# Kernel tuning notes

Measured on AMD Instinct MI355X. Metric: run time of the kernel, lower is better.

## Reference

```python
import jax, jax.numpy as jnp
import numpy as np

# Static problem configuration
NUM_GRAPHS = 64
NODES_PER_GRAPH = 2048          # divisible by OUT_H
NODE_EMB_DIM = 256              # divisible by OUT_W
COND_EMB_DIM = 64
OUT_H, OUT_W = 16, 8            # AdaptiveAvgPool2d output -> pooled dim H*W = 128
MLP_H = 256
BN_EPS = 1e-5


def setup_inputs() -> dict:
    key = jax.random.key(0)
    ks = jax.random.split(key, 8)
    N = NUM_GRAPHS * NODES_PER_GRAPH
    x = jax.random.normal(ks[0], (N, NODE_EMB_DIM), dtype=jnp.float32)
    # equal contiguous segments: node i belongs to graph i // NODES_PER_GRAPH
    batch = jnp.repeat(jnp.arange(NUM_GRAPHS, dtype=jnp.int64), NODES_PER_GRAPH)
    conditioner_z_ref = jax.random.normal(ks[1], (N, COND_EMB_DIM), dtype=jnp.float32)
    mlp_in = COND_EMB_DIM + OUT_H * OUT_W
    W1 = jax.random.normal(ks[2], (mlp_in, MLP_H), dtype=jnp.float32) / np.sqrt(mlp_in)
    b1 = jnp.zeros((MLP_H,), dtype=jnp.float32)
    gamma = jnp.ones((MLP_H,), dtype=jnp.float32)
    beta = jnp.zeros((MLP_H,), dtype=jnp.float32)
    W2 = jax.random.normal(ks[3], (MLP_H, 3), dtype=jnp.float32) / np.sqrt(MLP_H)
    b2 = jnp.zeros((3,), dtype=jnp.float32)
    return {"x": x, "batch": batch, "conditioner_z_ref": conditioner_z_ref,
            "W1": W1, "b1": b1, "gamma": gamma, "beta": beta, "W2": W2, "b2": b2}


def _adaptive_pool(x):
    # x: [N_total, D] with equal contiguous segments of NODES_PER_GRAPH rows per graph.
    # AdaptiveAvgPool2d((OUT_H, OUT_W)) on each [n, D] "image"; since n % OUT_H == 0
    # and D % OUT_W == 0 the adaptive bins are uniform -> exact reshape-mean.
    B = x.shape[0] // NODES_PER_GRAPH
    xg = x.reshape(B, OUT_H, NODES_PER_GRAPH // OUT_H, OUT_W, NODE_EMB_DIM // OUT_W)
    pooled = xg.mean(axis=(2, 4))                 # [B, OUT_H, OUT_W]
    return pooled.reshape(B, OUT_H * OUT_W)       # [B, H*W]


def reference(x, batch, conditioner_z_ref, W1, b1, gamma, beta, W2, b2):
    batch_pooled = _adaptive_pool(x)                          # [B, H*W]
    gathered = batch_pooled[batch]                            # [N, H*W]
    h = jnp.concatenate([conditioner_z_ref, gathered], axis=1)  # [N, cond + H*W]
    # Linear -> BatchNorm1d (training-mode batch stats, biased var) -> GELU (exact)
    h = h @ W1 + b1                                           # [N, MLP_H]
    mean = h.mean(axis=0)
    var = h.var(axis=0)
    h = (h - mean) * jax.lax.rsqrt(var + BN_EPS) * gamma + beta
    h = jax.nn.gelu(h, approximate=False)
    return h @ W2 + b2                                        # [N, 3]
```

## Files before the change

### kernel.cpp

```cpp
#include <hip/hip_runtime.h>
#include <math.h>

#define NG    64
#define NPG   2048
#define NTOT  (NG*NPG)
#define ZD    64
#define PD    128
#define MH    256

typedef __attribute__((ext_vector_type(8))) short bf16x8;
typedef __attribute__((ext_vector_type(4))) float f32x4;

__device__ __forceinline__ unsigned short f2bf(float f){
  unsigned u = __float_as_uint(f);
  unsigned r = u + 0x7FFFu + ((u >> 16) & 1u);
  return (unsigned short)(r >> 16);
}
__device__ __forceinline__ float bf2f(unsigned short s){
  return __uint_as_float(((unsigned)s) << 16);
}
__device__ __forceinline__ float gelu_f(float x){
  float u = x * x;
  float a = fmaf(0.044715f, u, 1.0f);
  float e = __builtin_amdgcn_exp2f(-2.3022083f * x * a);
  return x * __builtin_amdgcn_rcpf(1.0f + e);
}

__launch_bounds__(256)
__global__ void k1_pool_zstat(const float* __restrict__ x, const float* __restrict__ z,
                              float* __restrict__ pooled, float* __restrict__ St,
                              float* __restrict__ C){
  __shared__ __align__(16) unsigned short s_zt[64 * 264];
  __shared__ float s_cred[4096];
  int tid = threadIdx.x;

  if (blockIdx.x >= 256){
    int bi = blockIdx.x - 256;
    int b  = bi >> 4;
    int oh = bi & 15;
    int c4 = tid & 63;
    int rq = tid >> 6;
    const float4* x4 = (const float4*)x;
    size_t base = (size_t)(b * NPG + oh * 128) * 64;
    float4 acc = make_float4(0.f, 0.f, 0.f, 0.f);
    #pragma unroll 8
    for (int i = 0; i < 32; i++){
      float4 v = x4[base + (size_t)(rq + i * 4) * 64 + c4];
      acc.x += v.x; acc.y += v.y; acc.z += v.z; acc.w += v.w;
    }
    s_cred[tid] = acc.x + acc.y + acc.z + acc.w;
    __syncthreads();
    if (tid < 8){
      float s = 0.f;
      #pragma unroll
      for (int w = 0; w < 4; w++)
        #pragma unroll
        for (int j = 0; j < 8; j++)
          s += s_cred[w * 64 + tid * 8 + j];
      pooled[b * PD + oh * 8 + tid] = s * (1.0f / 4096.0f);
    }
    return;
  }

  int blk = blockIdx.x;
  int g = blk >> 2, q4 = blk & 3;
  int lane = tid & 63, wave = tid >> 6;
  int col = lane & 15, quad = lane >> 4;
  const float4* z4 = (const float4*)z + ((size_t)g * 2048 + q4 * 512) * 16;
  int d4 = col;
  int mg = quad;

  f32x4 acc[4][4];
  #pragma unroll
  for (int a = 0; a < 4; a++)
    #pragma unroll
    for (int b = 0; b < 4; b++) acc[a][b] = (f32x4)(0.f);
  float s0 = 0.f, s1 = 0.f, s2 = 0.f, s3 = 0.f;

  for (int ch = 0; ch < 2; ch++){
    #pragma unroll
    for (int rd = 0; rd < 4; rd++){
      int m0 = rd * 64 + wave * 16 + mg * 4;
      const float4* src = z4 + ch * 4096 + m0 * 16 + d4;
      float4 v0 = src[0];
      float4 v1 = src[16];
      float4 v2 = src[32];
      float4 v3 = src[48];
      s0 += v0.x + v1.x + v2.x + v3.x;
      s1 += v0.y + v1.y + v2.y + v3.y;
      s2 += v0.z + v1.z + v2.z + v3.z;
      s3 += v0.w + v1.w + v2.w + v3.w;
      int slot = m0 >> 3;
      int sub  = m0 & 4;
      int d0 = d4 * 4;
      {
        int d = d0 + 0; int ss = slot ^ ((d >> 3) & 7);
        ushort4 w = make_ushort4(f2bf(v0.x), f2bf(v1.x), f2bf(v2.x), f2bf(v3.x));
        *(ushort4*)&s_zt[d * 264 + ss * 8 + sub] = w;
      }
      {
        int d = d0 + 1; int ss = slot ^ ((d >> 3) & 7);
        ushort4 w = make_ushort4(f2bf(v0.y), f2bf(v1.y), f2bf(v2.y), f2bf(v3.y));
        *(ushort4*)&s_zt[d * 264 + ss * 8 + sub] = w;
      }
      {
        int d = d0 + 2; int ss = slot ^ ((d >> 3) & 7);
        ushort4 w = make_ushort4(f2bf(v0.z), f2bf(v1.z), f2bf(v2.z), f2bf(v3.z));
        *(ushort4*)&s_zt[d * 264 + ss * 8 + sub] = w;
      }
      {
        int d = d0 + 3; int ss = slot ^ ((d >> 3) & 7);
        ushort4 w = make_ushort4(f2bf(v0.w), f2bf(v1.w), f2bf(v2.w), f2bf(v3.w));
        *(ushort4*)&s_zt[d * 264 + ss * 8 + sub] = w;
      }
    }
    __syncthreads();
    #pragma unroll
    for (int ks = 0; ks < 2; ks++){
      bf16x8 fr[4];
      #pragma unroll
      for (int t = 0; t < 4; t++){
        int row = t * 16 + col;
        int ss  = (wave * 8 + ks * 4 + quad) ^ ((row >> 3) & 7);
        fr[t] = *(const bf16x8*)&s_zt[row * 264 + ss * 8];
      }
      #pragma unroll
      for (int mt = 0; mt < 4; mt++)
        #pragma unroll
        for (int nt = 0; nt < 4; nt++)
          acc[mt][nt] = __builtin_amdgcn_mfma_f32_16x16x32_bf16(fr[mt], fr[nt], acc[mt][nt], 0, 0, 0);
    }
    __syncthreads();
  }

  s0 += __shfl_xor(s0, 16); s0 += __shfl_xor(s0, 32);
  s1 += __shfl_xor(s1, 16); s1 += __shfl_xor(s1, 32);
  s2 += __shfl_xor(s2, 16); s2 += __shfl_xor(s2, 32);
  s3 += __shfl_xor(s3, 16); s3 += __shfl_xor(s3, 32);
  if (quad == 0){
    atomicAdd(&St[(d4 * 4 + 0) * 64 + g], s0);
    atomicAdd(&St[(d4 * 4 + 1) * 64 + g], s1);
    atomicAdd(&St[(d4 * 4 + 2) * 64 + g], s2);
    atomicAdd(&St[(d4 * 4 + 3) * 64 + g], s3);
  }

  #pragma unroll
  for (int w = 0; w < 4; w++){
    if (wave == w){
      #pragma unroll
      for (int mt = 0; mt < 4; mt++)
        #pragma unroll
        for (int nt = 0; nt < 4; nt++)
          #pragma unroll
          for (int r = 0; r < 4; r++){
            int p = mt * 16 + quad * 4 + r;
            int qc = nt * 16 + col;
            if (w == 0) s_cred[p * 64 + qc]  = acc[mt][nt][r];
            else        s_cred[p * 64 + qc] += acc[mt][nt][r];
          }
    }
    __syncthreads();
  }
  for (int f = tid; f < 4096; f += 256)
    atomicAdd(&C[f], s_cred[f]);
}

__launch_bounds__(256)
__global__ void k2_stats(const float* __restrict__ pooled, const float* __restrict__ W1,
                         const float* __restrict__ b1, const float* __restrict__ gamma,
                         const float* __restrict__ beta, const float* __restrict__ C,
                         const float* __restrict__ St, float* __restrict__ Aj,
                         float* __restrict__ cprime, unsigned short* __restrict__ Wbf){
  __shared__ float pl[64 * 129];
  int tid = threadIdx.x;
  int jc = tid >> 6, lane = tid & 63;
  int j = blockIdx.x * 4 + jc;

  Wbf[(size_t)j * 64 + lane] = f2bf(W1[(size_t)lane * 256 + j]);

  for (int idx = tid; idx < 8192; idx += 256)
    pl[(idx >> 7) * 129 + (idx & 127)] = pooled[idx];
  __syncthreads();

  float g = b1[j];
  #pragma unroll 8
  for (int k = 0; k < 128; k++)
    g = fmaf(pl[lane * 129 + k], W1[(size_t)(ZD + k) * MH + j], g);

  float wl = W1[(size_t)lane * MH + j];
  float t1 = 0.f, t2 = 0.f;
  #pragma unroll
  for (int q = 0; q < 64; q++){
    float wq = __uint_as_float(__builtin_amdgcn_readlane(__float_as_uint(wl), q));
    t1 = fmaf(C [q * 64 + lane], wq, t1);
    t2 = fmaf(St[q * 64 + lane], wq, t2);
  }
  float v_wcw = wl * t1;
  float v_gs  = g * t2;
  float v_s   = t2;
  float v_g   = g;
  float v_g2  = g * g;
  #pragma unroll
  for (int off = 32; off; off >>= 1){
    v_wcw += __shfl_xor(v_wcw, off);
    v_gs  += __shfl_xor(v_gs , off);
    v_s   += __shfl_xor(v_s  , off);
    v_g   += __shfl_xor(v_g  , off);
    v_g2  += __shfl_xor(v_g2 , off);
  }
  const float invN = 1.0f / (float)NTOT;
  float mean = v_s * invN + v_g * (1.0f / 64.0f);
  float eh2  = v_wcw * invN + 2.0f * invN * v_gs + v_g2 * (1.0f / 64.0f);
  float var  = eh2 - mean * mean;
  float aj = gamma[j] * rsqrtf(var + 1e-5f);
  if (lane == 0) Aj[j] = aj;
  cprime[lane * MH + j] = fmaf(aj, g, beta[j] - aj * mean);
}

__launch_bounds__(256, 2)
__global__ void final_kernel(const float* __restrict__ z, const unsigned short* __restrict__ Wbf,
                             const float* __restrict__ Aj, const float* __restrict__ cp,
                             const float* __restrict__ W2, const float* __restrict__ b2,
                             float* __restrict__ out){
  __shared__ __align__(16) unsigned short zt[128 * 136];
  __shared__ float slab[2][384];
  int tid = threadIdx.x;
  int n0 = blockIdx.x * 128;
  int g = blockIdx.x >> 4;

  const float4* z4 = (const float4*)z + (size_t)n0 * 16;
  #pragma unroll
  for (int i = 0; i < 8; i++){
    int idx = tid + i * 256;
    int m = idx >> 4, d4 = idx & 15;
    float4 v = z4[idx];
    ushort4 h, l;
    h.x = f2bf(v.x); l.x = f2bf(v.x - bf2f(h.x));
    h.y = f2bf(v.y); l.y = f2bf(v.y - bf2f(h.y));
    h.z = f2bf(v.z); l.z = f2bf(v.z - bf2f(h.z));
    h.w = f2bf(v.w); l.w = f2bf(v.w - bf2f(h.w));
    *(ushort4*)&zt[m * 136 + d4 * 4]      = h;
    *(ushort4*)&zt[m * 136 + 64 + d4 * 4] = l;
  }
  __syncthreads();

  int lane = tid & 63, wave = tid >> 6;
  int wm = wave & 1, wn = wave >> 1;
  int col = lane & 15, quad = lane >> 4;
  int mbase = wm * 64, nbase = wn * 128;

  f32x4 acc[4][8];
  #pragma unroll
  for (int mt = 0; mt < 4; mt++)
    #pragma unroll
    for (int nt = 0; nt < 8; nt++) acc[mt][nt] = (f32x4)(0.f);

  #pragma unroll
  for (int ks = 0; ks < 4; ks++){
    int k0 = ks * 32;
    bf16x8 af[4];
    #pragma unroll
    for (int mt = 0; mt < 4; mt++)
      af[mt] = *(const bf16x8*)&zt[(mbase + mt * 16 + col) * 136 + k0 + quad * 8];
    #pragma unroll
    for (int nt = 0; nt < 8; nt++){
      bf16x8 bv = *(const bf16x8*)&Wbf[(size_t)(nbase + nt * 16 + col) * 64 + (ks & 1) * 32 + quad * 8];
      #pragma unroll
      for (int mt = 0; mt < 4; mt++)
        acc[mt][nt] = __builtin_amdgcn_mfma_f32_16x16x32_bf16(af[mt], bv, acc[mt][nt], 0, 0, 0);
    }
  }

  float aj[8], cj[8], w2a[8], w2b[8], w2c[8];
  #pragma unroll
  for (int nt = 0; nt < 8; nt++){
    int j = nbase + nt * 16 + col;
    aj[nt] = Aj[j];
    cj[nt] = cp[g * MH + j];
    w2a[nt] = W2[j * 3 + 0];
    w2b[nt] = W2[j * 3 + 1];
    w2c[nt] = W2[j * 3 + 2];
  }

  #pragma unroll
  for (int mt = 0; mt < 4; mt++){
    #pragma unroll
    for (int r = 0; r < 4; r++){
      float o0 = 0.f, o1 = 0.f, o2 = 0.f;
      #pragma unroll
      for (int nt = 0; nt < 8; nt++){
        float h  = fmaf(aj[nt], acc[mt][nt][r], cj[nt]);
        float ge = gelu_f(h);
        o0 = fmaf(ge, w2a[nt], o0);
        o1 = fmaf(ge, w2b[nt], o1);
        o2 = fmaf(ge, w2c[nt], o2);
      }
      #pragma unroll
      for (int off = 8; off; off >>= 1){
        o0 += __shfl_xor(o0, off);
        o1 += __shfl_xor(o1, off);
        o2 += __shfl_xor(o2, off);
      }
      if (col == 0){
        int node = mbase + mt * 16 + quad * 4 + r;
        slab[wn][node * 3 + 0] = o0;
        slab[wn][node * 3 + 1] = o1;
        slab[wn][node * 3 + 2] = o2;
      }
    }
  }
  __syncthreads();
  float b2v[3] = {b2[0], b2[1], b2[2]};
  for (int f = tid; f < 384; f += 256)
    out[(size_t)blockIdx.x * 384 + f] = slab[0][f] + slab[1][f] + b2v[f % 3];
}

extern "C" void kernel_launch(void* const* d_in, const int* in_sizes, int n_in,
                              void* d_out, int out_size, void* d_ws, size_t ws_size,
                              hipStream_t stream){
  (void)in_sizes; (void)n_in; (void)out_size; (void)ws_size;
  const float* x     = (const float*)d_in[0];
  const float* z     = (const float*)d_in[2];
  const float* W1    = (const float*)d_in[3];
  const float* b1    = (const float*)d_in[4];
  const float* gamma = (const float*)d_in[5];
  const float* beta  = (const float*)d_in[6];
  const float* W2    = (const float*)d_in[7];
  const float* b2    = (const float*)d_in[8];
  float* out = (float*)d_out;

  float* W = (float*)d_ws;
  float* pooled = W;
  float* St     = W + 8192;
  float* C      = W + 12288;
  float* Aj     = W + 16384;
  float* CP     = W + 16640;
  unsigned short* Wbf = (unsigned short*)(W + 33024);

  hipMemsetAsync((char*)d_ws + 8192 * 4, 0, 8192 * 4, stream);

  k1_pool_zstat<<<dim3(1280), dim3(256), 0, stream>>>(x, z, pooled, St, C);
  k2_stats     <<<dim3(64),   dim3(256), 0, stream>>>(pooled, W1, b1, gamma, beta, C, St, Aj, CP, Wbf);
  final_kernel <<<dim3(NTOT / 128), dim3(256), 0, stream>>>(z, Wbf, Aj, CP, W2, b2, out);
}
```

Baseline: 271.9 us.

## Fuse all stages into one cooperative persistent kernel with grid syncs

Replaces the memset plus three kernel launches with a single cooperative kernel of 512 blocks that zeroes accumulators, computes pooling and z statistics, derives BN coefficients, and runs the final MLP/GELU pass, separated by grid-wide syncs. It is meant to remove launch overhead and inter-kernel gaps. The final stage becomes a persistent loop over row tiles. The old path is kept as a fallback if the cooperative launch fails. Grid syncs, reduced parallelism per phase (only 64 blocks in the stats phase) and occupancy limits from the large shared buffer may offset the gains.

```diff
diff --git a/kernel.cpp b/kernel.cpp
--- a/kernel.cpp
+++ b/kernel.cpp
@@ -1,5 +1,8 @@
 #include <hip/hip_runtime.h>
+#include <hip/hip_cooperative_groups.h>
 #include <math.h>
+
+namespace cg = cooperative_groups;
 
 #define NG    64
 #define NPG   2048
@@ -24,6 +27,311 @@
   float a = fmaf(0.044715f, u, 1.0f);
   float e = __builtin_amdgcn_exp2f(-2.3022083f * x * a);
   return x * __builtin_amdgcn_rcpf(1.0f + e);
+}
+
+__launch_bounds__(256, 2)
+__global__ void fused_all(const float* __restrict__ x, const float* __restrict__ z,
+                          const float* __restrict__ W1, const float* __restrict__ b1,
+                          const float* __restrict__ gamma, const float* __restrict__ beta,
+                          const float* __restrict__ W2, const float* __restrict__ b2,
+                          float* __restrict__ pooled, float* __restrict__ St,
+                          float* __restrict__ C, float* __restrict__ Aj,
+                          float* __restrict__ cp, unsigned short* __restrict__ Wbf,
+                          float* __restrict__ out){
+  __shared__ __align__(16) unsigned char smem[50176];
+  cg::grid_group gg = cg::this_grid();
+  int tid = threadIdx.x;
+  int bid = blockIdx.x;
+  int nb  = gridDim.x;
+
+  if (bid < 32){
+    int i = bid * 256 + tid;
+    if (i < 4096) St[i] = 0.f;
+    else          C[i - 4096] = 0.f;
+  }
+  gg.sync();
+
+  {
+    unsigned short* s_zt = (unsigned short*)smem;
+    float* s_cred = (float*)(smem + 33792);
+
+    if (bid < 256){
+      int blk = bid;
+      int g = blk >> 2, q4 = blk & 3;
+      int lane = tid & 63, wave = tid >> 6;
+      int col = lane & 15, quad = lane >> 4;
+      const float4* z4 = (const float4*)z + ((size_t)g * 2048 + q4 * 512) * 16;
+      int d4 = col;
+      int mg = quad;
+
+      f32x4 acc[4][4];
+      #pragma unroll
+      for (int a = 0; a < 4; a++)
+        #pragma unroll
+        for (int b = 0; b < 4; b++) acc[a][b] = (f32x4)(0.f);
+      float s0 = 0.f, s1 = 0.f, s2 = 0.f, s3 = 0.f;
+
+      for (int ch = 0; ch < 2; ch++){
+        #pragma unroll
+        for (int rd = 0; rd < 4; rd++){
+          int m0 = rd * 64 + wave * 16 + mg * 4;
+          const float4* src = z4 + ch * 4096 + m0 * 16 + d4;
+          float4 v0 = src[0];
+          float4 v1 = src[16];
+          float4 v2 = src[32];
+          float4 v3 = src[48];
+          s0 += v0.x + v1.x + v2.x + v3.x;
+          s1 += v0.y + v1.y + v2.y + v3.y;
+          s2 += v0.z + v1.z + v2.z + v3.z;
+          s3 += v0.w + v1.w + v2.w + v3.w;
+          int slot = m0 >> 3;
+          int sub  = m0 & 4;
+          int d0 = d4 * 4;
+          {
+            int d = d0 + 0; int ss = slot ^ ((d >> 3) & 7);
+            ushort4 w = make_ushort4(f2bf(v0.x), f2bf(v1.x), f2bf(v2.x), f2bf(v3.x));
+            *(ushort4*)&s_zt[d * 264 + ss * 8 + sub] = w;
+          }
+          {
+            int d = d0 + 1; int ss = slot ^ ((d >> 3) & 7);
+            ushort4 w = make_ushort4(f2bf(v0.y), f2bf(v1.y), f2bf(v2.y), f2bf(v3.y));
+            *(ushort4*)&s_zt[d * 264 + ss * 8 + sub] = w;
+          }
+          {
+            int d = d0 + 2; int ss = slot ^ ((d >> 3) & 7);
+            ushort4 w = make_ushort4(f2bf(v0.z), f2bf(v1.z), f2bf(v2.z), f2bf(v3.z));
+            *(ushort4*)&s_zt[d * 264 + ss * 8 + sub] = w;
+          }
+          {
+            int d = d0 + 3; int ss = slot ^ ((d >> 3) & 7);
+            ushort4 w = make_ushort4(f2bf(v0.w), f2bf(v1.w), f2bf(v2.w), f2bf(v3.w));
+            *(ushort4*)&s_zt[d * 264 + ss * 8 + sub] = w;
+          }
+        }
+        __syncthreads();
+        #pragma unroll
+        for (int ks = 0; ks < 2; ks++){
+          bf16x8 fr[4];
+          #pragma unroll
+          for (int t = 0; t < 4; t++){
+            int row = t * 16 + col;
+            int ss  = (wave * 8 + ks * 4 + quad) ^ ((row >> 3) & 7);
+            fr[t] = *(const bf16x8*)&s_zt[row * 264 + ss * 8];
+          }
+          #pragma unroll
+          for (int mt = 0; mt < 4; mt++)
+            #pragma unroll
+            for (int nt = 0; nt < 4; nt++)
+              acc[mt][nt] = __builtin_amdgcn_mfma_f32_16x16x32_bf16(fr[mt], fr[nt], acc[mt][nt], 0, 0, 0);
+        }
+        __syncthreads();
+      }
+
+      s0 += __shfl_xor(s0, 16); s0 += __shfl_xor(s0, 32);
+      s1 += __shfl_xor(s1, 16); s1 += __shfl_xor(s1, 32);
+      s2 += __shfl_xor(s2, 16); s2 += __shfl_xor(s2, 32);
+      s3 += __shfl_xor(s3, 16); s3 += __shfl_xor(s3, 32);
+      if (quad == 0){
+        atomicAdd(&St[(d4 * 4 + 0) * 64 + g], s0);
+        atomicAdd(&St[(d4 * 4 + 1) * 64 + g], s1);
+        atomicAdd(&St[(d4 * 4 + 2) * 64 + g], s2);
+        atomicAdd(&St[(d4 * 4 + 3) * 64 + g], s3);
+      }
+
+      #pragma unroll
+      for (int w = 0; w < 4; w++){
+        if (wave == w){
+          #pragma unroll
+          for (int mt = 0; mt < 4; mt++)
+            #pragma unroll
+            for (int nt = 0; nt < 4; nt++)
+              #pragma unroll
+              for (int r = 0; r < 4; r++){
+                int p = mt * 16 + quad * 4 + r;
+                int qc = nt * 16 + col;
+                if (w == 0) s_cred[p * 64 + qc]  = acc[mt][nt][r];
+                else        s_cred[p * 64 + qc] += acc[mt][nt][r];
+              }
+        }
+        __syncthreads();
+      }
+      for (int f = tid; f < 4096; f += 256)
+        atomicAdd(&C[f], s_cred[f]);
+    }
+
+    int u0 = bid, nu = (bid < 256) ? 1 : 3;
+    for (int k = 0; k < nu; k++){
+      int bi = u0 + k * 256;
+      int b  = bi >> 4;
+      int oh = bi & 15;
+      int c4 = tid & 63;
+      int rq = tid >> 6;
+      const float4* x4 = (const float4*)x;
+      size_t base = (size_t)(b * NPG + oh * 128) * 64;
+      float4 acc = make_float4(0.f, 0.f, 0.f, 0.f);
+      #pragma unroll 8
+      for (int i = 0; i < 32; i++){
+        float4 v = x4[base + (size_t)(rq + i * 4) * 64 + c4];
+        acc.x += v.x; acc.y += v.y; acc.z += v.z; acc.w += v.w;
+      }
+      __syncthreads();
+      s_cred[tid] = acc.x + acc.y + acc.z + acc.w;
+      __syncthreads();
+      if (tid < 8){
+        float s = 0.f;
+        #pragma unroll
+        for (int w = 0; w < 4; w++)
+          #pragma unroll
+          for (int j = 0; j < 8; j++)
+            s += s_cred[w * 64 + tid * 8 + j];
+        pooled[b * PD + oh * 8 + tid] = s * (1.0f / 4096.0f);
+      }
+    }
+  }
+  gg.sync();
+
+  if (bid < 64){
+    float* pl = (float*)smem;
+    int jc = tid >> 6, lane = tid & 63;
+    int j = bid * 4 + jc;
+
+    Wbf[(size_t)j * 64 + lane] = f2bf(W1[(size_t)lane * 256 + j]);
+
+    for (int idx = tid; idx < 8192; idx += 256)
+      pl[(idx >> 7) * 129 + (idx & 127)] = pooled[idx];
+    __syncthreads();
+
+    float g = b1[j];
+    #pragma unroll 8
+    for (int k = 0; k < 128; k++)
+      g = fmaf(pl[lane * 129 + k], W1[(size_t)(ZD + k) * MH + j], g);
+
+    float wl = W1[(size_t)lane * MH + j];
+    float t1 = 0.f, t2 = 0.f;
+    #pragma unroll
+    for (int q = 0; q < 64; q++){
+      float wq = __uint_as_float(__builtin_amdgcn_readlane(__float_as_uint(wl), q));
+      t1 = fmaf(C [q * 64 + lane], wq, t1);
+      t2 = fmaf(St[q * 64 + lane], wq, t2);
+    }
+    float v_wcw = wl * t1;
+    float v_gs  = g * t2;
+    float v_s   = t2;
+    float v_g   = g;
+    float v_g2  = g * g;
+    #pragma unroll
+    for (int off = 32; off; off >>= 1){
+      v_wcw += __shfl_xor(v_wcw, off);
+      v_gs  += __shfl_xor(v_gs , off);
+      v_s   += __shfl_xor(v_s  , off);
+      v_g   += __shfl_xor(v_g  , off);
+      v_g2  += __shfl_xor(v_g2 , off);
+    }
+    const float invN = 1.0f / (float)NTOT;
+    float mean = v_s * invN + v_g * (1.0f / 64.0f);
+    float eh2  = v_wcw * invN + 2.0f * invN * v_gs + v_g2 * (1.0f / 64.0f);
+    float var  = eh2 - mean * mean;
+    float aj = gamma[j] * rsqrtf(var + 1e-5f);
+    if (lane == 0) Aj[j] = aj;
+    cp[lane * MH + j] = fmaf(aj, g, beta[j] - aj * mean);
+  }
+  gg.sync();
+
+  {
+    unsigned short* zt = (unsigned short*)smem;
+    float* slab = (float*)(smem + 34816);
+    int lane = tid & 63, wave = tid >> 6;
+    int wm = wave & 1, wn = wave >> 1;
+    int col = lane & 15, quad = lane >> 4;
+    int mbase = wm * 64, nbase = wn * 128;
+
+    for (int u = bid; u < 1024; u += nb){
+      int n0 = u * 128;
+      int g = u >> 4;
+
+      const float4* z4 = (const float4*)z + (size_t)n0 * 16;
+      __syncthreads();
+      #pragma unroll
+      for (int i = 0; i < 8; i++){
+        int idx = tid + i * 256;
+        int m = idx >> 4, d4 = idx & 15;
+        float4 v = z4[idx];
+        ushort4 h, l;
+        h.x = f2bf(v.x); l.x = f2bf(v.x - bf2f(h.x));
+        h.y = f2bf(v.y); l.y = f2bf(v.y - bf2f(h.y));
+        h.z = f2bf(v.z); l.z = f2bf(v.z - bf2f(h.z));
+        h.w = f2bf(v.w); l.w = f2bf(v.w - bf2f(h.w));
+        *(ushort4*)&zt[m * 136 + d4 * 4]      = h;
+        *(ushort4*)&zt[m * 136 + 64 + d4 * 4] = l;
+      }
+      __syncthreads();
+
+      f32x4 acc[4][8];
+      #pragma unroll
+      for (int mt = 0; mt < 4; mt++)
+        #pragma unroll
+        for (int nt = 0; nt < 8; nt++) acc[mt][nt] = (f32x4)(0.f);
+
+      #pragma unroll
+      for (int ks = 0; ks < 4; ks++){
+        int k0 = ks * 32;
+        bf16x8 af[4];
+        #pragma unroll
+        for (int mt = 0; mt < 4; mt++)
+          af[mt] = *(const bf16x8*)&zt[(mbase + mt * 16 + col) * 136 + k0 + quad * 8];
+        #pragma unroll
+        for (int nt = 0; nt < 8; nt++){
+          bf16x8 bv = *(const bf16x8*)&Wbf[(size_t)(nbase + nt * 16 + col) * 64 + (ks & 1) * 32 + quad * 8];
+          #pragma unroll
+          for (int mt = 0; mt < 4; mt++)
+            acc[mt][nt] = __builtin_amdgcn_mfma_f32_16x16x32_bf16(af[mt], bv, acc[mt][nt], 0, 0, 0);
+        }
+      }
+
+      float aj[8], cj[8], w2a[8], w2b[8], w2c[8];
+      #pragma unroll
+      for (int nt = 0; nt < 8; nt++){
+        int j = nbase + nt * 16 + col;
+        aj[nt] = Aj[j];
+        cj[nt] = cp[g * MH + j];
+        w2a[nt] = W2[j * 3 + 0];
+        w2b[nt] = W2[j * 3 + 1];
+        w2c[nt] = W2[j * 3 + 2];
+      }
+
+      #pragma unroll
+      for (int mt = 0; mt < 4; mt++){
+        #pragma unroll
+        for (int r = 0; r < 4; r++){
+          float o0 = 0.f, o1 = 0.f, o2 = 0.f;
+          #pragma unroll
+          for (int nt = 0; nt < 8; nt++){
+            float h  = fmaf(aj[nt], acc[mt][nt][r], cj[nt]);
+            float ge = gelu_f(h);
+            o0 = fmaf(ge, w2a[nt], o0);
+            o1 = fmaf(ge, w2b[nt], o1);
+            o2 = fmaf(ge, w2c[nt], o2);
+          }
+          #pragma unroll
+          for (int off = 8; off; off >>= 1){
+            o0 += __shfl_xor(o0, off);
+            o1 += __shfl_xor(o1, off);
+            o2 += __shfl_xor(o2, off);
+          }
+          if (col == 0){
+            int node = mbase + mt * 16 + quad * 4 + r;
+            slab[wn * 384 + node * 3 + 0] = o0;
+            slab[wn * 384 + node * 3 + 1] = o1;
+            slab[wn * 384 + node * 3 + 2] = o2;
+          }
+        }
+      }
+      __syncthreads();
+      float b2v[3] = {b2[0], b2[1], b2[2]};
+      for (int f = tid; f < 384; f += 256)
+        out[(size_t)u * 384 + f] = slab[f] + slab[384 + f] + b2v[f % 3];
+    }
+  }
 }
 
 __launch_bounds__(256)
@@ -337,9 +645,15 @@
   float* CP     = W + 16640;
   unsigned short* Wbf = (unsigned short*)(W + 33024);
 
-  hipMemsetAsync((char*)d_ws + 8192 * 4, 0, 8192 * 4, stream);
-
-  k1_pool_zstat<<<dim3(1280), dim3(256), 0, stream>>>(x, z, pooled, St, C);
-  k2_stats     <<<dim3(64),   dim3(256), 0, stream>>>(pooled, W1, b1, gamma, beta, C, St, Aj, CP, Wbf);
-  final_kernel <<<dim3(NTOT / 128), dim3(256), 0, stream>>>(z, Wbf, Aj, CP, W2, b2, out);
-}
+  void* args[] = {(void*)&x, (void*)&z, (void*)&W1, (void*)&b1, (void*)&gamma,
+                  (void*)&beta, (void*)&W2, (void*)&b2, (void*)&pooled, (void*)&St,
+                  (void*)&C, (void*)&Aj, (void*)&CP, (void*)&Wbf, (void*)&out};
+  hipError_t err = hipLaunchCooperativeKernel((const void*)fused_all, dim3(512), dim3(256),
+                                              args, 0, stream);
+  if (err != hipSuccess){
+    hipMemsetAsync((char*)d_ws + 8192 * 4, 0, 8192 * 4, stream);
+    k1_pool_zstat<<<dim3(1280), dim3(256), 0, stream>>>(x, z, pooled, St, C);
+    k2_stats     <<<dim3(64),   dim3(256), 0, stream>>>(pooled, W1, b1, gamma, beta, C, St, Aj, CP, Wbf);
+    final_kernel <<<dim3(NTOT / 128), dim3(256), 0, stream>>>(z, Wbf, Aj, CP, W2, b2, out);
+  }
+}
```

After: 458.7 us. 68.7% more time.
